# Optimization experiments

Measured on AMD Instinct MI355X. Metric: run time of the kernel, lower is better.

Reference implementation:

```python
import jax, jax.numpy as jnp
import numpy as np

B, S, H, L = 64, 512, 1024, 9


def setup_inputs() -> dict:
    key = jax.random.key(0)
    k1, k2, k3, k4 = jax.random.split(key, 4)
    sequence_output = jax.random.normal(k1, (B, S, H), dtype=jnp.float32)
    valid_mask = jax.random.randint(k2, (B, S), 0, 2, dtype=jnp.int32)
    # classifier params (Dense(num_labels), TruncatedNormal(stddev=0.02) ~ normal here)
    W = jax.random.normal(k3, (H, L), dtype=jnp.float32) * 0.02
    b = jnp.zeros((L,), dtype=jnp.float32)
    return {"sequence_output": sequence_output, "valid_mask": valid_mask, "W": W, "b": b}


def _compact_valid(sequence_output, valid_mask):
    # Stable-sort tokens so valid (mask==1) tokens come first in original order,
    # then zero-pad the tail -- vectorized equivalent of the per-token Python loop.
    Bq, Sq, _ = sequence_output.shape
    pos = jnp.arange(Sq, dtype=jnp.int32)[None, :]                 # [1,S]
    sort_key = (1 - valid_mask) * Sq + pos                         # invalid pushed back, stable
    order = jnp.argsort(sort_key, axis=1)                          # [B,S]
    gathered = jnp.take_along_axis(sequence_output, order[:, :, None], axis=1)
    n_valid = jnp.sum(valid_mask, axis=1, keepdims=True)           # [B,1]
    keep = (pos < n_valid)[:, :, None]                             # [B,S,1]
    return jnp.where(keep, gathered, jnp.zeros((), sequence_output.dtype))


def reference(sequence_output, valid_mask, W, b):
    valid_output = _compact_valid(sequence_output, valid_mask)     # [B,S,H]
    # dropout is identity at inference (training=False)
    logits = jnp.einsum("bsh,hl->bsl", valid_output, W) + b
    return jax.nn.softmax(logits, axis=-1)
```

## Files before the change

### kernel.cpp

```cpp
#include <hip/hip_runtime.h>
#include <hip/hip_bf16.h>

#define BB 64
#define SS 512
#define HH 1024
#define LL 9

template <int CTRL>
__device__ __forceinline__ float dpp_add(float v) {
    int s = __builtin_bit_cast(int, v);
    int r = __builtin_amdgcn_update_dpp(0, s, CTRL, 0xF, 0xF, true);
    return v + __builtin_bit_cast(float, r);
}

__global__ __launch_bounds__(256) void fused_ner_kernel(
    const float* __restrict__ x, const int* __restrict__ mask,
    const float* __restrict__ W, const float* __restrict__ bias,
    float* __restrict__ out) {
    __shared__ __align__(16) float Wl[HH * LL];
    __shared__ int gidx_sh[SS];
    __shared__ int wsum[4];
    __shared__ float bsh[LL];
    __shared__ float obuf[64 * LL];

    const int tid  = threadIdx.x;
    const int bat  = blockIdx.x & 63;
    const int blk  = blockIdx.x >> 6;
    const int lane = tid & 63;
    const int wv_  = tid >> 6;

    #pragma unroll
    for (int i = 0; i < 9; ++i) {
        const int f4 = i * 256 + tid;
        __builtin_amdgcn_global_load_lds(
            (const __attribute__((address_space(1))) void*)(W + f4 * 4),
            (__attribute__((address_space(3))) void*)(&Wl[f4 * 4]),
            16, 0, 0);
    }
    if (tid < LL) bsh[tid] = bias[tid];

    const int2 mm = reinterpret_cast<const int2*>(mask + bat * SS)[tid];
    const int m0 = mm.x, m1 = mm.y;
    const int s = m0 + m1;
    int incl = s;
    #pragma unroll
    for (int off = 1; off < 64; off <<= 1) {
        int u = __shfl_up(incl, off, 64);
        if (lane >= off) incl += u;
    }
    if (lane == 63) wsum[wv_] = incl;
    __syncthreads();
    int wbase = 0;
    #pragma unroll
    for (int i = 0; i < 4; ++i) if (i < wv_) wbase += wsum[i];
    const int nv = wsum[0] + wsum[1] + wsum[2] + wsum[3];
    const int excl = incl - s + wbase;
    if (m0) gidx_sh[excl] = 2 * tid;
    if (m1) gidx_sh[excl + m0] = 2 * tid + 1;
    __syncthreads();

    const int jbeg = (blk * nv) >> 3;
    const int jend = ((blk + 1) * nv) >> 3;
    const int nwork = jend - jbeg;
    const int npad = SS - nv;
    const int pbeg = nv + ((blk * npad) >> 3);
    const int pend = nv + (((blk + 1) * npad) >> 3);

    const int g = lane >> 4;
    const int k = lane & 15;
    const int G = wv_ * 4 + g;

    float acc[4][LL];
    #pragma unroll
    for (int r = 0; r < 4; ++r)
        #pragma unroll
        for (int l = 0; l < LL; ++l) acc[r][l] = 0.f;

    float sc[4];
    const float4* xr[4];
    #pragma unroll
    for (int r = 0; r < 4; ++r) {
        const int j = jbeg + G * 4 + r;
        const bool valid = (j < jend);
        sc[r] = valid ? 1.f : 0.f;
        const int src = valid ? gidx_sh[j] : 0;
        xr[r] = reinterpret_cast<const float4*>(x + ((size_t)bat * SS + src) * HH);
    }

    if (G * 4 < nwork || (g == 0 && wv_ == 0 && nwork > 0)) {  }
    if (wv_ * 16 < nwork) {
        float4 xv[4][4];
        #pragma unroll
        for (int c = 0; c < 3; ++c)
            #pragma unroll
            for (int r = 0; r < 4; ++r) xv[c][r] = xr[r][c * 16 + k];

        #pragma unroll 4
        for (int c = 0; c < 16; ++c) {
            const int nc = (c + 3) & 15;
            #pragma unroll
            for (int r = 0; r < 4; ++r) xv[nc & 3][r] = xr[r][nc * 16 + k];

            float4 wb[9];
            const float* wp = &Wl[(c * 16 + k) * 36];
            #pragma unroll
            for (int j2 = 0; j2 < 9; ++j2)
                wb[j2] = *reinterpret_cast<const float4*>(wp + j2 * 4);
            const float* wf = reinterpret_cast<const float*>(wb);

            #pragma unroll
            for (int l = 0; l < LL; ++l) {
                #pragma unroll
                for (int r = 0; r < 4; ++r) {
                    const float4 xvv = xv[c & 3][r];
                    acc[r][l] += xvv.x * wf[0 * 9 + l] + xvv.y * wf[1 * 9 + l]
                               + xvv.z * wf[2 * 9 + l] + xvv.w * wf[3 * 9 + l];
                }
            }
        }
        #pragma unroll
        for (int r = 0; r < 4; ++r)
            #pragma unroll
            for (int l = 0; l < LL; ++l) {
                float v = acc[r][l];
                v = dpp_add<0x111>(v);
                v = dpp_add<0x112>(v);
                v = dpp_add<0x114>(v);
                v = dpp_add<0x118>(v);
                acc[r][l] = v;
            }

        if (k == 15) {
            #pragma unroll
            for (int r = 0; r < 4; ++r) {
                float lg[LL];
                float mx = -3.0e38f;
                #pragma unroll
                for (int l = 0; l < LL; ++l) {
                    lg[l] = acc[r][l] * sc[r] + bsh[l];
                    mx = fmaxf(mx, lg[l]);
                }
                float ssum = 0.f;
                #pragma unroll
                for (int l = 0; l < LL; ++l) { lg[l] = __expf(lg[l] - mx); ssum += lg[l]; }
                const float inv = 1.f / ssum;
                const int lp = G * 4 + r;
                #pragma unroll
                for (int l = 0; l < LL; ++l) obuf[lp * LL + l] = lg[l] * inv;
            }
        }
    }

    float bs[LL];
    float mxb = -3.0e38f;
    #pragma unroll
    for (int l = 0; l < LL; ++l) { bs[l] = bsh[l]; mxb = fmaxf(mxb, bs[l]); }
    float sb = 0.f;
    #pragma unroll
    for (int l = 0; l < LL; ++l) { bs[l] = __expf(bs[l] - mxb); sb += bs[l]; }
    const float invb = 1.f / sb;

    __syncthreads();

    const size_t vbase = ((size_t)bat * SS + jbeg) * LL;
    for (int t = tid; t < nwork * LL; t += 256) out[vbase + t] = obuf[t];

    const size_t pbase = ((size_t)bat * SS + pbeg) * LL;
    const int pn = (pend - pbeg) * LL;
    for (int t = tid; t < pn; t += 256) {
        const int row = t / LL;
        const int l   = t - row * LL;
        out[pbase + t] = bs[l] * invb;
    }
}

extern "C" void kernel_launch(void* const* d_in, const int* in_sizes, int n_in,
                              void* d_out, int out_size, void* d_ws, size_t ws_size,
                              hipStream_t stream) {
    const float* x    = (const float*)d_in[0];
    const int*   mask = (const int*)d_in[1];
    const float* W    = (const float*)d_in[2];
    const float* bias = (const float*)d_in[3];
    float* out = (float*)d_out;

    fused_ner_kernel<<<BB * 8, 256, 0, stream>>>(x, mask, W, bias, out);
}
```

Baseline: 24.87 us.

## Process rows with full wavefront per 4 rows in looped passes

Restructures work so each wavefront handles 4 rows at a time across the full 64-lane width of the hidden dimension, looping up to 4 passes, instead of 16 rows per wave split into 16-lane groups. All x loads for a pass are issued up front, replacing the rolling prefetch, and the reduction gains two cross-group shuffles. The softmax is then spread across the four 16-lane groups rather than run serially for 4 rows in one lane. The aim is to skip work for idle rows when a block has fewer valid rows and to shorten the serial softmax tail. The cost is that passes run serially with less memory-level parallelism inside each pass.

Result: faster. 24.14 us (-2.9%).

```diff
diff --git a/kernel.cpp b/kernel.cpp
--- a/kernel.cpp
+++ b/kernel.cpp
@@ -68,41 +68,39 @@
 
     const int g = lane >> 4;
     const int k = lane & 15;
-    const int G = wv_ * 4 + g;
 
-    float acc[4][LL];
-    #pragma unroll
-    for (int r = 0; r < 4; ++r)
+    #pragma unroll 1
+    for (int pass = 0; pass < 4; ++pass) {
+        const int lp0 = pass * 16 + wv_ * 4;
+        if (lp0 >= nwork) break;
+
+        float sc[4];
+        const float4* xr[4];
         #pragma unroll
-        for (int l = 0; l < LL; ++l) acc[r][l] = 0.f;
+        for (int r = 0; r < 4; ++r) {
+            const int j = jbeg + lp0 + r;
+            const bool valid = (j < jend);
+            sc[r] = valid ? 1.f : 0.f;
+            const int src = gidx_sh[valid ? j : jbeg];
+            xr[r] = reinterpret_cast<const float4*>(x + ((size_t)bat * SS + src) * HH);
+        }
 
-    float sc[4];
-    const float4* xr[4];
-    #pragma unroll
-    for (int r = 0; r < 4; ++r) {
-        const int j = jbeg + G * 4 + r;
-        const bool valid = (j < jend);
-        sc[r] = valid ? 1.f : 0.f;
-        const int src = valid ? gidx_sh[j] : 0;
-        xr[r] = reinterpret_cast<const float4*>(x + ((size_t)bat * SS + src) * HH);
-    }
+        float4 xq[4][4];
+        #pragma unroll
+        for (int i = 0; i < 4; ++i)
+            #pragma unroll
+            for (int r = 0; r < 4; ++r) xq[r][i] = xr[r][i * 64 + lane];
 
-    if (G * 4 < nwork || (g == 0 && wv_ == 0 && nwork > 0)) {  }
-    if (wv_ * 16 < nwork) {
-        float4 xv[4][4];
+        float acc[4][LL];
         #pragma unroll
-        for (int c = 0; c < 3; ++c)
+        for (int r = 0; r < 4; ++r)
             #pragma unroll
-            for (int r = 0; r < 4; ++r) xv[c][r] = xr[r][c * 16 + k];
+            for (int l = 0; l < LL; ++l) acc[r][l] = 0.f;
 
-        #pragma unroll 4
-        for (int c = 0; c < 16; ++c) {
-            const int nc = (c + 3) & 15;
-            #pragma unroll
-            for (int r = 0; r < 4; ++r) xv[nc & 3][r] = xr[r][nc * 16 + k];
-
+        #pragma unroll
+        for (int i = 0; i < 4; ++i) {
             float4 wb[9];
-            const float* wp = &Wl[(c * 16 + k) * 36];
+            const float* wp = &Wl[(i * 64 + lane) * 36];
             #pragma unroll
             for (int j2 = 0; j2 < 9; ++j2)
                 wb[j2] = *reinterpret_cast<const float4*>(wp + j2 * 4);
@@ -112,12 +110,13 @@
             for (int l = 0; l < LL; ++l) {
                 #pragma unroll
                 for (int r = 0; r < 4; ++r) {
-                    const float4 xvv = xv[c & 3][r];
+                    const float4 xvv = xq[r][i];
                     acc[r][l] += xvv.x * wf[0 * 9 + l] + xvv.y * wf[1 * 9 + l]
                                + xvv.z * wf[2 * 9 + l] + xvv.w * wf[3 * 9 + l];
                 }
             }
         }
+
         #pragma unroll
         for (int r = 0; r < 4; ++r)
             #pragma unroll
@@ -127,27 +126,30 @@
                 v = dpp_add<0x112>(v);
                 v = dpp_add<0x114>(v);
                 v = dpp_add<0x118>(v);
+                v += __shfl_xor(v, 16, 64);
+                v += __shfl_xor(v, 32, 64);
                 acc[r][l] = v;
             }
 
+        float lg[LL];
+        #pragma unroll
+        for (int l = 0; l < LL; ++l) {
+            float v = acc[0][l] * sc[0];
+            if (g == 1) v = acc[1][l] * sc[1];
+            if (g == 2) v = acc[2][l] * sc[2];
+            if (g == 3) v = acc[3][l] * sc[3];
+            lg[l] = v + bsh[l];
+        }
+        float mx = -3.0e38f;
+        #pragma unroll
+        for (int l = 0; l < LL; ++l) mx = fmaxf(mx, lg[l]);
+        float ssum = 0.f;
+        #pragma unroll
+        for (int l = 0; l < LL; ++l) { lg[l] = __expf(lg[l] - mx); ssum += lg[l]; }
+        const float inv = 1.f / ssum;
         if (k == 15) {
             #pragma unroll
-            for (int r = 0; r < 4; ++r) {
-                float lg[LL];
-                float mx = -3.0e38f;
-                #pragma unroll
-                for (int l = 0; l < LL; ++l) {
-                    lg[l] = acc[r][l] * sc[r] + bsh[l];
-                    mx = fmaxf(mx, lg[l]);
-                }
-                float ssum = 0.f;
-                #pragma unroll
-                for (int l = 0; l < LL; ++l) { lg[l] = __expf(lg[l] - mx); ssum += lg[l]; }
-                const float inv = 1.f / ssum;
-                const int lp = G * 4 + r;
-                #pragma unroll
-                for (int l = 0; l < LL; ++l) obuf[lp * LL + l] = lg[l] * inv;
-            }
+            for (int l = 0; l < LL; ++l) obuf[(lp0 + g) * LL + l] = lg[l] * inv;
         }
     }
 
```
